# Optimization experiments

Hardware: AMD Instinct MI355X
Metric: run time of the kernel (lower is better)

Reference implementation:

```python
import jax, jax.numpy as jnp
import numpy as np

N_HEADS, D_MODEL, D_HEAD = 16, 1024, 64
INIT_STD = 0.02


def setup_inputs() -> dict:
    key = jax.random.key(0)
    ks = jax.random.split(key, 5)
    x = jax.random.normal(ks[0], (4, 2048, D_MODEL), dtype=jnp.float32)
    W_Q = jax.random.normal(ks[1], (N_HEADS, D_MODEL, D_HEAD), dtype=jnp.float32) * INIT_STD
    W_K = jax.random.normal(ks[2], (N_HEADS, D_MODEL, D_HEAD), dtype=jnp.float32) * INIT_STD
    W_V = jax.random.normal(ks[3], (N_HEADS, D_MODEL, D_HEAD), dtype=jnp.float32) * INIT_STD
    W_O = jax.random.normal(ks[4], (N_HEADS, D_HEAD, D_MODEL), dtype=jnp.float32) * INIT_STD
    b_Q = jnp.zeros((N_HEADS, D_HEAD), dtype=jnp.float32)
    b_K = jnp.zeros((N_HEADS, D_HEAD), dtype=jnp.float32)
    b_V = jnp.zeros((N_HEADS, D_HEAD), dtype=jnp.float32)
    b_O = jnp.zeros((D_MODEL,), dtype=jnp.float32)
    return {"normalized_resid_pre": x, "W_Q": W_Q, "W_K": W_K, "W_V": W_V,
            "W_O": W_O, "b_Q": b_Q, "b_K": b_K, "b_V": b_V, "b_O": b_O}


def reference(normalized_resid_pre, W_Q, W_K, W_V, W_O, b_Q, b_K, b_V, b_O):
    x = normalized_resid_pre  # [b, s, d_model]
    q = jnp.einsum('bsm,hmd->bshd', x, W_Q) + b_Q  # [b, s, h, d_head]
    k = jnp.einsum('bsm,hmd->bshd', x, W_K) + b_K
    v = jnp.einsum('bsm,hmd->bshd', x, W_V) + b_V
    scores = jnp.einsum('bqhd,bkhd->bhqk', q, k) / jnp.sqrt(jnp.float32(D_HEAD))
    S = x.shape[1]
    causal = jnp.tril(jnp.ones((S, S), dtype=bool))  # keep key_pos <= query_pos
    scores = jnp.where(causal, scores, jnp.finfo(scores.dtype).min)
    pattern = jax.nn.softmax(scores, axis=-1)  # [b, h, q, k]
    z = jnp.einsum('bhqk,bkhd->bqhd', pattern, v)
    attn_out = jnp.einsum('bqhd,hdm->bqm', z, W_O) + b_O
    return attn_out
```

## Files before the change

kernel.cpp:

```cpp
#include <hip/hip_runtime.h>
#include <hip/hip_bf16.h>
#include <math.h>

typedef __bf16 bf16_t;
typedef bf16_t bf16x8 __attribute__((ext_vector_type(8)));
typedef float f32x4 __attribute__((ext_vector_type(4)));

#define BB 4
#define SS 2048
#define HH 16
#define DMODEL 1024
#define DHEAD 64

#define QSCALE 0.18033688011112042f

__device__ inline unsigned short f2bf(float f) {
    union { __hip_bfloat16 h; unsigned short u; } cvt;
    cvt.h = __float2bfloat16(f);
    return cvt.u;
}

__device__ __forceinline__ void gll16(const unsigned short* g, unsigned short* l) {
    __builtin_amdgcn_global_load_lds(
        (const __attribute__((address_space(1))) unsigned int*)(g),
        (__attribute__((address_space(3))) unsigned int*)(l), 16, 0, 0);
}


__global__ void pack_x(const float* __restrict__ x, unsigned short* __restrict__ xb) {
    int i = blockIdx.x * 256 + threadIdx.x;
    const float4 v = ((const float4*)x)[i];
    unsigned short o[4] = { f2bf(v.x), f2bf(v.y), f2bf(v.z), f2bf(v.w) };
    *(uint2*)(xb + 4 * (size_t)i) = *(uint2*)o;
}

__global__ void pack_wqkv(const float* __restrict__ wq, const float* __restrict__ wk,
                          const float* __restrict__ wv, unsigned short* __restrict__ out) {
    int idx = blockIdx.x * 256 + threadIdx.x;
    int k  = idx & 1023;
    int n  = idx >> 10;
    int mat = n >> 10;
    int n1 = n & 1023;
    int h = n1 >> 6, d = n1 & 63;
    const float* w = (mat == 0) ? wq : (mat == 1) ? wk : wv;
    out[idx] = f2bf(w[(h << 16) + (k << 6) + d]);
}

__global__ void pack_wo(const float* __restrict__ wo, unsigned short* __restrict__ out) {
    int idx = blockIdx.x * 256 + threadIdx.x;
    int k = idx & 1023, n = idx >> 10;
    out[idx] = f2bf(wo[(k << 10) + n]);
}


__global__ __launch_bounds__(256) void gemm_qkv(
    const unsigned short* __restrict__ xb,
    const unsigned short* __restrict__ wT,
    const float* __restrict__ bq, const float* __restrict__ bk, const float* __restrict__ bv,
    unsigned short* __restrict__ qws, unsigned short* __restrict__ kws,
    unsigned short* __restrict__ vtw)
{
    __shared__ __align__(16) unsigned short lA[128 * 32];
    __shared__ __align__(16) unsigned short lB[128 * 32];
    const int t = threadIdx.x;
    const int lane = t & 63;
    const int w = t >> 6;
    const int quad = lane >> 4;
    const int l15 = lane & 15;
    const int n0 = blockIdx.x * 128;
    const int m0 = blockIdx.y * 128;
    const int wm = (w >> 1) * 64;
    const int wn = (w & 1) * 64;
    const int mat = n0 >> 10;

    f32x4 acc[4][4] = {};

    const int srow = w * 16 + (lane >> 2);
    const int scol = (lane & 3) * 8;
    const unsigned short* Ag0 = xb + (size_t)(m0 + srow) * 1024 + scol;
    const unsigned short* Ag1 = Ag0 + (size_t)64 * 1024;
    const unsigned short* Bg0 = wT + (size_t)(n0 + srow) * 1024 + scol;
    const unsigned short* Bg1 = Bg0 + (size_t)64 * 1024;
    unsigned short* lA0 = lA + (w * 16) * 32;
    unsigned short* lA1 = lA + (64 + w * 16) * 32;
    unsigned short* lB0 = lB + (w * 16) * 32;
    unsigned short* lB1 = lB + (64 + w * 16) * 32;

    if (mat != 2) {
        for (int kt = 0; kt < 1024; kt += 32) {
            __syncthreads();
            gll16(Ag0 + kt, lA0);
            gll16(Ag1 + kt, lA1);
            gll16(Bg0 + kt, lB0);
            gll16(Bg1 + kt, lB1);
            __syncthreads();
            bf16x8 af[4], bfr[4];
#pragma unroll
            for (int i = 0; i < 4; i++) {
                af[i]  = *(const bf16x8*)(lA + (wm + i * 16 + l15) * 32 + quad * 8);
                bfr[i] = *(const bf16x8*)(lB + (wn + i * 16 + l15) * 32 + quad * 8);
            }
#pragma unroll
            for (int i = 0; i < 4; i++)
#pragma unroll
                for (int j = 0; j < 4; j++)
                    acc[i][j] = __builtin_amdgcn_mfma_f32_16x16x32_bf16(bfr[j], af[i], acc[i][j], 0, 0, 0);
        }
        const int b = m0 >> 11;
        const float* bias_p = (mat == 0) ? bq : bk;
        const float scale = (mat == 0) ? QSCALE : 1.0f;
        unsigned short* dst = (mat == 0) ? qws : kws;
#pragma unroll
        for (int j = 0; j < 4; j++) {
            const int noff = wn + j * 16 + quad * 4;
            const int h = noff >> 6;
            const int hglob = ((n0 & 1023) >> 6) + h;
            const int dbase = noff & 63;
            const float4 bv4 = *(const float4*)(bias_p + hglob * 64 + dbase);
            const float bias_r[4] = { bv4.x, bv4.y, bv4.z, bv4.w };
#pragma unroll
            for (int i = 0; i < 4; i++) {
                const int s = (m0 & 2047) + wm + i * 16 + l15;
                unsigned short pk[4];
#pragma unroll
                for (int r = 0; r < 4; r++) pk[r] = f2bf((acc[i][j][r] + bias_r[r]) * scale);
                *(uint2*)(dst + (size_t)((b * 16 + hglob) * 2048 + s) * 64 + dbase) = *(uint2*)pk;
            }
        }
    } else {
        for (int kt = 0; kt < 1024; kt += 32) {
            __syncthreads();
            gll16(Ag0 + kt, lA0);
            gll16(Ag1 + kt, lA1);
            gll16(Bg0 + kt, lB0);
            gll16(Bg1 + kt, lB1);
            __syncthreads();
            bf16x8 af[4], bfr[4];
#pragma unroll
            for (int i = 0; i < 4; i++) {
                af[i]  = *(const bf16x8*)(lA + (wm + i * 16 + l15) * 32 + quad * 8);
                bfr[i] = *(const bf16x8*)(lB + (wn + i * 16 + l15) * 32 + quad * 8);
            }
#pragma unroll
            for (int i = 0; i < 4; i++)
#pragma unroll
                for (int j = 0; j < 4; j++)
                    acc[i][j] = __builtin_amdgcn_mfma_f32_16x16x32_bf16(af[i], bfr[j], acc[i][j], 0, 0, 0);
        }
        const int b = m0 >> 11;
#pragma unroll
        for (int j = 0; j < 4; j++) {
            const int n1 = (n0 & 1023) + wn + j * 16 + l15;
            const int h = n1 >> 6, d = n1 & 63;
            const float bias = bv[h * 64 + d];
#pragma unroll
            for (int i = 0; i < 4; i++) {
                const int s0 = (m0 & 2047) + wm + i * 16 + quad * 4;
                unsigned short pk[4];
#pragma unroll
                for (int r = 0; r < 4; r++) pk[r] = f2bf(acc[i][j][r] + bias);
                *(uint2*)(vtw + ((size_t)(b * 16 + h) * 64 + d) * 2048 + s0) = *(uint2*)pk;
            }
        }
    }
}


__global__ __launch_bounds__(256) void attn3(
    const unsigned short* __restrict__ qws,
    const unsigned short* __restrict__ kws,
    const unsigned short* __restrict__ vtw,
    unsigned short* __restrict__ zb)
{
    __shared__ __align__(16) unsigned short Ks[64 * 64];
    __shared__ __align__(16) unsigned short Vs[64 * 64];
    __shared__ __align__(16) unsigned short Ps[4 * 16 * 64];

    const int t = threadIdx.x;
    const int lane = t & 63;
    const int w = t >> 6;
    const int quad = lane >> 4;
    const int l15 = lane & 15;
    const int hi = l15 >> 3;
    const int lo = l15 & 7;

    const int qt = 31 - (blockIdx.x >> 6);
    const int bh = blockIdx.x & 63;
    const int q0 = qt * 64;
    const int qbase = q0 + w * 16;
    const size_t base = (size_t)bh * SS * DHEAD;
    const unsigned short* Q = qws + base;
    const unsigned short* K = kws + base;
    const unsigned short* Vt = vtw + base;

    bf16x8 qf0 = *(const bf16x8*)(Q + (size_t)(qbase + l15) * 64 + quad * 8);
    bf16x8 qf1 = *(const bf16x8*)(Q + (size_t)(qbase + l15) * 64 + 32 + quad * 8);

    f32x4 o[4] = {};
    float lsum[4] = {0.f, 0.f, 0.f, 0.f};
    unsigned short* Pw = Ps + w * 16 * 64;

    const int sr = t >> 2;
    const int g0 = t & 3;
    const int sw0 = ((g0 ^ (sr & 7)) << 3);
    const int sw1 = (((g0 + 4) ^ (sr & 7)) << 3);
    unsigned short* ksw = Ks + sr * 64;
    unsigned short* vsw = Vs + sr * 64;
    const unsigned short* Kg = K + (size_t)sr * 64 + g0 * 8;
    const unsigned short* Vg = Vt + (size_t)sr * 2048 + g0 * 8;

    const int gq0 = ((quad ^ lo) << 3);
    const int gq1 = (((quad + 4) ^ lo) << 3);

    const int nch = qt + 1;

    uint4 kr0 = *(const uint4*)(Kg);
    uint4 kr1 = *(const uint4*)(Kg + 32);
    uint4 vr0 = *(const uint4*)(Vg);
    uint4 vr1 = *(const uint4*)(Vg + 32);

    for (int c = 0; c < nch; c++) {
        __builtin_amdgcn_sched_barrier(0);
        __builtin_amdgcn_s_barrier();
        *(uint4*)(ksw + sw0) = kr0;
        *(uint4*)(ksw + sw1) = kr1;
        *(uint4*)(vsw + sw0) = vr0;
        *(uint4*)(vsw + sw1) = vr1;
        if (c + 1 < nch) {
            const unsigned short* kp = Kg + (size_t)(c + 1) * 64 * 64;
            const unsigned short* vp = Vg + (size_t)(c + 1) * 64;
            kr0 = *(const uint4*)(kp);
            kr1 = *(const uint4*)(kp + 32);
            vr0 = *(const uint4*)(vp);
            vr1 = *(const uint4*)(vp + 32);
        }
        asm volatile("s_waitcnt lgkmcnt(0)" ::: "memory");
        __builtin_amdgcn_s_barrier();
        __builtin_amdgcn_sched_barrier(0);

        f32x4 s[4];
        __builtin_amdgcn_s_setprio(1);
#pragma unroll
        for (int sub = 0; sub < 4; sub++) {
            const unsigned short* kr = Ks + (sub * 16 + l15) * 64;
            bf16x8 kf0 = *(const bf16x8*)(kr + gq0);
            bf16x8 kf1 = *(const bf16x8*)(kr + gq1);
            f32x4 sv = {};
            sv = __builtin_amdgcn_mfma_f32_16x16x32_bf16(qf0, kf0, sv, 0, 0, 0);
            sv = __builtin_amdgcn_mfma_f32_16x16x32_bf16(qf1, kf1, sv, 0, 0, 0);
            s[sub] = sv;
        }
        __builtin_amdgcn_s_setprio(0);

        const int kb = c * 64;
        if (c == nch - 1) {
            const int qg = qbase + quad * 4;
#pragma unroll
            for (int sub = 0; sub < 4; sub++) {
                const int key = kb + sub * 16 + l15;
#pragma unroll
                for (int r = 0; r < 4; r++) {
                    float p = (key > qg + r) ? 0.f : exp2f(s[sub][r]);
                    lsum[r] += p;
                    const int q = quad * 4 + r;
                    Pw[q * 64 + (((sub * 2 + hi) ^ (q & 7)) << 3) + lo] = f2bf(p);
                }
            }
        } else {
#pragma unroll
            for (int sub = 0; sub < 4; sub++)
#pragma unroll
                for (int r = 0; r < 4; r++) {
                    float p = exp2f(s[sub][r]);
                    lsum[r] += p;
                    const int q = quad * 4 + r;
                    Pw[q * 64 + (((sub * 2 + hi) ^ (q & 7)) << 3) + lo] = f2bf(p);
                }
        }
        asm volatile("s_waitcnt lgkmcnt(0)" ::: "memory");
        bf16x8 pf0 = *(const bf16x8*)(Pw + l15 * 64 + gq0);
        bf16x8 pf1 = *(const bf16x8*)(Pw + l15 * 64 + gq1);
        __builtin_amdgcn_s_setprio(1);
#pragma unroll
        for (int dt = 0; dt < 4; dt++) {
            const unsigned short* vrp = Vs + (dt * 16 + l15) * 64;
            bf16x8 vf0 = *(const bf16x8*)(vrp + gq0);
            bf16x8 vf1 = *(const bf16x8*)(vrp + gq1);
            o[dt] = __builtin_amdgcn_mfma_f32_16x16x32_bf16(vf0, pf0, o[dt], 0, 0, 0);
            o[dt] = __builtin_amdgcn_mfma_f32_16x16x32_bf16(vf1, pf1, o[dt], 0, 0, 0);
        }
        __builtin_amdgcn_s_setprio(0);
    }

#pragma unroll
    for (int r = 0; r < 4; r++) {
        float v = lsum[r];
        v += __shfl_xor(v, 1);
        v += __shfl_xor(v, 2);
        v += __shfl_xor(v, 4);
        v += __shfl_xor(v, 8);
        lsum[r] = v;
    }
    const int srcl = (l15 >> 2) << 4;
    float t0 = __shfl(lsum[0], srcl);
    float t1 = __shfl(lsum[1], srcl);
    float t2 = __shfl(lsum[2], srcl);
    float t3 = __shfl(lsum[3], srcl);
    const int rr = l15 & 3;
    float den = (rr == 0) ? t0 : (rr == 1) ? t1 : (rr == 2) ? t2 : t3;
    const float inv = 1.0f / den;

    const int b = bh >> 4, h = bh & 15;
    const int q = qbase + l15;
    unsigned short* zrow = zb + (size_t)(b * 2048 + q) * 1024 + h * 64 + quad * 4;
#pragma unroll
    for (int dt = 0; dt < 4; dt++) {
        unsigned short pk[4];
#pragma unroll
        for (int r = 0; r < 4; r++) pk[r] = f2bf(o[dt][r] * inv);
        *(uint2*)(zrow + dt * 16) = *(uint2*)pk;
    }
}


__global__ __launch_bounds__(256) void gemm_out(
    const unsigned short* __restrict__ zb,
    const unsigned short* __restrict__ wT,
    const float* __restrict__ bo,
    float* __restrict__ out)
{
    __shared__ __align__(16) unsigned short lA[128 * 32];
    __shared__ __align__(16) unsigned short lB[128 * 32];
    const int t = threadIdx.x;
    const int lane = t & 63;
    const int w = t >> 6;
    const int quad = lane >> 4;
    const int l15 = lane & 15;
    const int n0 = blockIdx.x * 128;
    const int m0 = blockIdx.y * 128;
    const int wm = (w >> 1) * 64;
    const int wn = (w & 1) * 64;

    f32x4 acc[4][4] = {};

    const int srow = w * 16 + (lane >> 2);
    const int scol = (lane & 3) * 8;
    const unsigned short* Ag0 = zb + (size_t)(m0 + srow) * 1024 + scol;
    const unsigned short* Ag1 = Ag0 + (size_t)64 * 1024;
    const unsigned short* Bg0 = wT + (size_t)(n0 + srow) * 1024 + scol;
    const unsigned short* Bg1 = Bg0 + (size_t)64 * 1024;
    unsigned short* lA0 = lA + (w * 16) * 32;
    unsigned short* lA1 = lA + (64 + w * 16) * 32;
    unsigned short* lB0 = lB + (w * 16) * 32;
    unsigned short* lB1 = lB + (64 + w * 16) * 32;

    for (int kt = 0; kt < 1024; kt += 32) {
        __syncthreads();
        gll16(Ag0 + kt, lA0);
        gll16(Ag1 + kt, lA1);
        gll16(Bg0 + kt, lB0);
        gll16(Bg1 + kt, lB1);
        __syncthreads();
        bf16x8 af[4], bfr[4];
#pragma unroll
        for (int i = 0; i < 4; i++) {
            af[i]  = *(const bf16x8*)(lA + (wm + i * 16 + l15) * 32 + quad * 8);
            bfr[i] = *(const bf16x8*)(lB + (wn + i * 16 + l15) * 32 + quad * 8);
        }
#pragma unroll
        for (int i = 0; i < 4; i++)
#pragma unroll
            for (int j = 0; j < 4; j++)
                acc[i][j] = __builtin_amdgcn_mfma_f32_16x16x32_bf16(bfr[j], af[i], acc[i][j], 0, 0, 0);
    }

#pragma unroll
    for (int j = 0; j < 4; j++) {
        const int nbase = n0 + wn + j * 16 + quad * 4;
        const float4 bv4 = *(const float4*)(bo + nbase);
#pragma unroll
        for (int i = 0; i < 4; i++) {
            const int s = m0 + wm + i * 16 + l15;
            float4 v;
            v.x = acc[i][j][0] + bv4.x;
            v.y = acc[i][j][1] + bv4.y;
            v.z = acc[i][j][2] + bv4.z;
            v.w = acc[i][j][3] + bv4.w;
            *(float4*)(out + (size_t)s * 1024 + nbase) = v;
        }
    }
}


extern "C" void kernel_launch(void* const* d_in, const int* in_sizes, int n_in,
                              void* d_out, int out_size, void* d_ws, size_t ws_size,
                              hipStream_t stream) {
    const float* x  = (const float*)d_in[0];
    const float* WQ = (const float*)d_in[1];
    const float* WK = (const float*)d_in[2];
    const float* WV = (const float*)d_in[3];
    const float* WO = (const float*)d_in[4];
    const float* bQ = (const float*)d_in[5];
    const float* bK = (const float*)d_in[6];
    const float* bV = (const float*)d_in[7];
    const float* bO = (const float*)d_in[8];
    float* out = (float*)d_out;

    char* ws = (char*)d_ws;
    unsigned short* xb   = (unsigned short*)ws;
    unsigned short* wqkv = (unsigned short*)(ws + (16u << 20));
    unsigned short* woT  = (unsigned short*)(ws + (22u << 20));
    unsigned short* qws  = (unsigned short*)(ws + (24u << 20));
    unsigned short* kws  = (unsigned short*)(ws + (40u << 20));
    unsigned short* vtw  = (unsigned short*)(ws + (56u << 20));
    unsigned short* zbuf = xb;

    pack_x<<<8192, 256, 0, stream>>>(x, xb);
    pack_wqkv<<<(3072 * 1024) / 256, 256, 0, stream>>>(WQ, WK, WV, wqkv);
    pack_wo<<<(1024 * 1024) / 256, 256, 0, stream>>>(WO, woT);
    gemm_qkv<<<dim3(24, 64), 256, 0, stream>>>(xb, wqkv, bQ, bK, bV, qws, kws, vtw);
    attn3<<<2048, 256, 0, stream>>>(qws, kws, vtw, zbuf);
    gemm_out<<<dim3(8, 64), 256, 0, stream>>>(zbuf, woT, bO, out);
}
```

Baseline: 303.3 us.

## Merge pack kernels with tiled transpose and transpose S in attention

Replaces the three separate bf16 pack kernels with a single launch. The weight transposes now go through a 64x64 shared-memory tile, so both the reads and writes are coalesced instead of scalar gathers. In attention, the QK^T MFMA operands are swapped so each lane holds one query row. This turns the P stores into 8-byte vector writes and shrinks the row-sum reduction to two cross-lane shuffles. The cost is more branching in the combined pack kernel and a new swizzle layout for P that has to stay consistent with the readback pattern.

```diff
diff --git a/kernel.cpp b/kernel.cpp
--- a/kernel.cpp
+++ b/kernel.cpp
@@ -27,29 +27,59 @@
 }
 
 
-__global__ void pack_x(const float* __restrict__ x, unsigned short* __restrict__ xb) {
-    int i = blockIdx.x * 256 + threadIdx.x;
-    const float4 v = ((const float4*)x)[i];
-    unsigned short o[4] = { f2bf(v.x), f2bf(v.y), f2bf(v.z), f2bf(v.w) };
-    *(uint2*)(xb + 4 * (size_t)i) = *(uint2*)o;
-}
-
-__global__ void pack_wqkv(const float* __restrict__ wq, const float* __restrict__ wk,
-                          const float* __restrict__ wv, unsigned short* __restrict__ out) {
-    int idx = blockIdx.x * 256 + threadIdx.x;
-    int k  = idx & 1023;
-    int n  = idx >> 10;
-    int mat = n >> 10;
-    int n1 = n & 1023;
-    int h = n1 >> 6, d = n1 & 63;
-    const float* w = (mat == 0) ? wq : (mat == 1) ? wk : wv;
-    out[idx] = f2bf(w[(h << 16) + (k << 6) + d]);
-}
-
-__global__ void pack_wo(const float* __restrict__ wo, unsigned short* __restrict__ out) {
-    int idx = blockIdx.x * 256 + threadIdx.x;
-    int k = idx & 1023, n = idx >> 10;
-    out[idx] = f2bf(wo[(k << 10) + n]);
+__global__ void pack_all(const float* __restrict__ x,
+                         const float* __restrict__ wq, const float* __restrict__ wk,
+                         const float* __restrict__ wv, const float* __restrict__ wo,
+                         unsigned short* __restrict__ xb, unsigned short* __restrict__ wqkv,
+                         unsigned short* __restrict__ woT) {
+    __shared__ float tile[64][65];
+    const int t = threadIdx.x;
+    const int bid = blockIdx.x;
+    if (bid < 8192) {
+        int i = bid * 256 + t;
+        const float4 v = ((const float4*)x)[i];
+        unsigned short o[4] = { f2bf(v.x), f2bf(v.y), f2bf(v.z), f2bf(v.w) };
+        *(uint2*)(xb + 4 * (size_t)i) = *(uint2*)o;
+        return;
+    }
+    const float* sbase;
+    int sstride;
+    unsigned short* dbase;
+    if (bid < 8192 + 768) {
+        int b2 = bid - 8192;
+        int mat = b2 >> 8, rem = b2 & 255;
+        int h = rem >> 4, mt = rem & 15;
+        const float* wsrc = (mat == 0) ? wq : (mat == 1) ? wk : wv;
+        sbase = wsrc + (h << 16) + ((mt * 64) << 6);
+        sstride = 64;
+        dbase = wqkv + (size_t)(mat * 1024 + h * 64) * 1024 + mt * 64;
+    } else {
+        int b3 = bid - 8960;
+        int kt = b3 >> 4, nt = b3 & 15;
+        sbase = wo + (size_t)(kt * 64) * 1024 + nt * 64;
+        sstride = 1024;
+        dbase = woT + (size_t)(nt * 64) * 1024 + kt * 64;
+    }
+    const int rr = t >> 4;
+    const int c4 = (t & 15) * 4;
+#pragma unroll
+    for (int i = 0; i < 4; i++) {
+        const int m = rr + 16 * i;
+        const float4 v = *(const float4*)(sbase + (size_t)m * sstride + c4);
+        tile[m][c4 + 0] = v.x;
+        tile[m][c4 + 1] = v.y;
+        tile[m][c4 + 2] = v.z;
+        tile[m][c4 + 3] = v.w;
+    }
+    __syncthreads();
+#pragma unroll
+    for (int i = 0; i < 4; i++) {
+        const int d = rr + 16 * i;
+        unsigned short pk[4];
+#pragma unroll
+        for (int j = 0; j < 4; j++) pk[j] = f2bf(tile[c4 + j][d]);
+        *(uint2*)(dbase + (size_t)d * 1024 + c4) = *(uint2*)pk;
+    }
 }
 
 
@@ -166,163 +196,6 @@
 }
 
 
-__global__ __launch_bounds__(256) void attn3(
-    const unsigned short* __restrict__ qws,
-    const unsigned short* __restrict__ kws,
-    const unsigned short* __restrict__ vtw,
-    unsigned short* __restrict__ zb)
-{
-    __shared__ __align__(16) unsigned short Ks[64 * 64];
-    __shared__ __align__(16) unsigned short Vs[64 * 64];
-    __shared__ __align__(16) unsigned short Ps[4 * 16 * 64];
-
-    const int t = threadIdx.x;
-    const int lane = t & 63;
-    const int w = t >> 6;
-    const int quad = lane >> 4;
-    const int l15 = lane & 15;
-    const int hi = l15 >> 3;
-    const int lo = l15 & 7;
-
-    const int qt = 31 - (blockIdx.x >> 6);
-    const int bh = blockIdx.x & 63;
-    const int q0 = qt * 64;
-    const int qbase = q0 + w * 16;
-    const size_t base = (size_t)bh * SS * DHEAD;
-    const unsigned short* Q = qws + base;
-    const unsigned short* K = kws + base;
-    const unsigned short* Vt = vtw + base;
-
-    bf16x8 qf0 = *(const bf16x8*)(Q + (size_t)(qbase + l15) * 64 + quad * 8);
-    bf16x8 qf1 = *(const bf16x8*)(Q + (size_t)(qbase + l15) * 64 + 32 + quad * 8);
-
-    f32x4 o[4] = {};
-    float lsum[4] = {0.f, 0.f, 0.f, 0.f};
-    unsigned short* Pw = Ps + w * 16 * 64;
-
-    const int sr = t >> 2;
-    const int g0 = t & 3;
-    const int sw0 = ((g0 ^ (sr & 7)) << 3);
-    const int sw1 = (((g0 + 4) ^ (sr & 7)) << 3);
-    unsigned short* ksw = Ks + sr * 64;
-    unsigned short* vsw = Vs + sr * 64;
-    const unsigned short* Kg = K + (size_t)sr * 64 + g0 * 8;
-    const unsigned short* Vg = Vt + (size_t)sr * 2048 + g0 * 8;
-
-    const int gq0 = ((quad ^ lo) << 3);
-    const int gq1 = (((quad + 4) ^ lo) << 3);
-
-    const int nch = qt + 1;
-
-    uint4 kr0 = *(const uint4*)(Kg);
-    uint4 kr1 = *(const uint4*)(Kg + 32);
-    uint4 vr0 = *(const uint4*)(Vg);
-    uint4 vr1 = *(const uint4*)(Vg + 32);
-
-    for (int c = 0; c < nch; c++) {
-        __builtin_amdgcn_sched_barrier(0);
-        __builtin_amdgcn_s_barrier();
-        *(uint4*)(ksw + sw0) = kr0;
-        *(uint4*)(ksw + sw1) = kr1;
-        *(uint4*)(vsw + sw0) = vr0;
-        *(uint4*)(vsw + sw1) = vr1;
-        if (c + 1 < nch) {
-            const unsigned short* kp = Kg + (size_t)(c + 1) * 64 * 64;
-            const unsigned short* vp = Vg + (size_t)(c + 1) * 64;
-            kr0 = *(const uint4*)(kp);
-            kr1 = *(const uint4*)(kp + 32);
-            vr0 = *(const uint4*)(vp);
-            vr1 = *(const uint4*)(vp + 32);
-        }
-        asm volatile("s_waitcnt lgkmcnt(0)" ::: "memory");
-        __builtin_amdgcn_s_barrier();
-        __builtin_amdgcn_sched_barrier(0);
-
-        f32x4 s[4];
-        __builtin_amdgcn_s_setprio(1);
-#pragma unroll
-        for (int sub = 0; sub < 4; sub++) {
-            const unsigned short* kr = Ks + (sub * 16 + l15) * 64;
-            bf16x8 kf0 = *(const bf16x8*)(kr + gq0);
-            bf16x8 kf1 = *(const bf16x8*)(kr + gq1);
-            f32x4 sv = {};
-            sv = __builtin_amdgcn_mfma_f32_16x16x32_bf16(qf0, kf0, sv, 0, 0, 0);
-            sv = __builtin_amdgcn_mfma_f32_16x16x32_bf16(qf1, kf1, sv, 0, 0, 0);
-            s[sub] = sv;
-        }
-        __builtin_amdgcn_s_setprio(0);
-
-        const int kb = c * 64;
-        if (c == nch - 1) {
-            const int qg = qbase + quad * 4;
-#pragma unroll
-            for (int sub = 0; sub < 4; sub++) {
-                const int key = kb + sub * 16 + l15;
-#pragma unroll
-                for (int r = 0; r < 4; r++) {
-                    float p = (key > qg + r) ? 0.f : exp2f(s[sub][r]);
-                    lsum[r] += p;
-                    const int q = quad * 4 + r;
-                    Pw[q * 64 + (((sub * 2 + hi) ^ (q & 7)) << 3) + lo] = f2bf(p);
-                }
-            }
-        } else {
-#pragma unroll
-            for (int sub = 0; sub < 4; sub++)
-#pragma unroll
-                for (int r = 0; r < 4; r++) {
-                    float p = exp2f(s[sub][r]);
-                    lsum[r] += p;
-                    const int q = quad * 4 + r;
-                    Pw[q * 64 + (((sub * 2 + hi) ^ (q & 7)) << 3) + lo] = f2bf(p);
-                }
-        }
-        asm volatile("s_waitcnt lgkmcnt(0)" ::: "memory");
-        bf16x8 pf0 = *(const bf16x8*)(Pw + l15 * 64 + gq0);
-        bf16x8 pf1 = *(const bf16x8*)(Pw + l15 * 64 + gq1);
-        __builtin_amdgcn_s_setprio(1);
-#pragma unroll
-        for (int dt = 0; dt < 4; dt++) {
-            const unsigned short* vrp = Vs + (dt * 16 + l15) * 64;
-            bf16x8 vf0 = *(const bf16x8*)(vrp + gq0);
-            bf16x8 vf1 = *(const bf16x8*)(vrp + gq1);
-            o[dt] = __builtin_amdgcn_mfma_f32_16x16x32_bf16(vf0, pf0, o[dt], 0, 0, 0);
-            o[dt] = __builtin_amdgcn_mfma_f32_16x16x32_bf16(vf1, pf1, o[dt], 0, 0, 0);
-        }
-        __builtin_amdgcn_s_setprio(0);
-    }
-
-#pragma unroll
-    for (int r = 0; r < 4; r++) {
-        float v = lsum[r];
-        v += __shfl_xor(v, 1);
-        v += __shfl_xor(v, 2);
-        v += __shfl_xor(v, 4);
-        v += __shfl_xor(v, 8);
-        lsum[r] = v;
-    }
-    const int srcl = (l15 >> 2) << 4;
-    float t0 = __shfl(lsum[0], srcl);
-    float t1 = __shfl(lsum[1], srcl);
-    float t2 = __shfl(lsum[2], srcl);
-    float t3 = __shfl(lsum[3], srcl);
-    const int rr = l15 & 3;
-    float den = (rr == 0) ? t0 : (rr == 1) ? t1 : (rr == 2) ? t2 : t3;
-    const float inv = 1.0f / den;
-
-    const int b = bh >> 4, h = bh & 15;
-    const int q = qbase + l15;
-    unsigned short* zrow = zb + (size_t)(b * 2048 + q) * 1024 + h * 64 + quad * 4;
-#pragma unroll
-    for (int dt = 0; dt < 4; dt++) {
-        unsigned short pk[4];
-#pragma unroll
-        for (int r = 0; r < 4; r++) pk[r] = f2bf(o[dt][r] * inv);
-        *(uint2*)(zrow + dt * 16) = *(uint2*)pk;
-    }
-}
-
-
 __global__ __launch_bounds__(256) void gemm_out(
     const unsigned short* __restrict__ zb,
     const unsigned short* __restrict__ wT,
@@ -392,6 +265,160 @@
 }
 
 
+__global__ __launch_bounds__(256) void attn3(
+    const unsigned short* __restrict__ qws,
+    const unsigned short* __restrict__ kws,
+    const unsigned short* __restrict__ vtw,
+    unsigned short* __restrict__ zb)
+{
+    __shared__ __align__(16) unsigned short Ks[64 * 64];
+    __shared__ __align__(16) unsigned short Vs[64 * 64];
+    __shared__ __align__(16) unsigned short Ps[4 * 16 * 64];
+
+    const int t = threadIdx.x;
+    const int lane = t & 63;
+    const int w = t >> 6;
+    const int quad = lane >> 4;
+    const int l15 = lane & 15;
+    const int lo = l15 & 7;
+
+    const int qt = 31 - (blockIdx.x >> 6);
+    const int bh = blockIdx.x & 63;
+    const int q0 = qt * 64;
+    const int qbase = q0 + w * 16;
+    const size_t base = (size_t)bh * SS * DHEAD;
+    const unsigned short* Q = qws + base;
+    const unsigned short* K = kws + base;
+    const unsigned short* Vt = vtw + base;
+
+    bf16x8 qf0 = *(const bf16x8*)(Q + (size_t)(qbase + l15) * 64 + quad * 8);
+    bf16x8 qf1 = *(const bf16x8*)(Q + (size_t)(qbase + l15) * 64 + 32 + quad * 8);
+
+    f32x4 o[4] = {};
+    float lsum = 0.f;
+    unsigned short* Pw = Ps + w * 16 * 64;
+
+    const int sr = t >> 2;
+    const int g0 = t & 3;
+    const int sw0 = ((g0 ^ (sr & 7)) << 3);
+    const int sw1 = (((g0 + 4) ^ (sr & 7)) << 3);
+    unsigned short* ksw = Ks + sr * 64;
+    unsigned short* vsw = Vs + sr * 64;
+    const unsigned short* Kg = K + (size_t)sr * 64 + g0 * 8;
+    const unsigned short* Vg = Vt + (size_t)sr * 2048 + g0 * 8;
+
+    const int gq0 = ((quad ^ lo) << 3);
+    const int gq1 = (((quad + 4) ^ lo) << 3);
+
+    unsigned short* pwr = Pw + l15 * 64;
+    unsigned short* pws0 = pwr + (((0 + quad) ^ (lo << 1)) << 2);
+    unsigned short* pws1 = pwr + (((4 + quad) ^ (lo << 1)) << 2);
+    unsigned short* pws2 = pwr + (((8 + quad) ^ (lo << 1)) << 2);
+    unsigned short* pws3 = pwr + (((12 + quad) ^ (lo << 1)) << 2);
+
+    const int nch = qt + 1;
+
+    uint4 kr0 = *(const uint4*)(Kg);
+    uint4 kr1 = *(const uint4*)(Kg + 32);
+    uint4 vr0 = *(const uint4*)(Vg);
+    uint4 vr1 = *(const uint4*)(Vg + 32);
+
+    for (int c = 0; c < nch; c++) {
+        __builtin_amdgcn_sched_barrier(0);
+        __builtin_amdgcn_s_barrier();
+        *(uint4*)(ksw + sw0) = kr0;
+        *(uint4*)(ksw + sw1) = kr1;
+        *(uint4*)(vsw + sw0) = vr0;
+        *(uint4*)(vsw + sw1) = vr1;
+        if (c + 1 < nch) {
+            const unsigned short* kp = Kg + (size_t)(c + 1) * 64 * 64;
+            const unsigned short* vp = Vg + (size_t)(c + 1) * 64;
+            kr0 = *(const uint4*)(kp);
+            kr1 = *(const uint4*)(kp + 32);
+            vr0 = *(const uint4*)(vp);
+            vr1 = *(const uint4*)(vp + 32);
+        }
+        asm volatile("s_waitcnt lgkmcnt(0)" ::: "memory");
+        __builtin_amdgcn_s_barrier();
+        __builtin_amdgcn_sched_barrier(0);
+
+        f32x4 s[4];
+        __builtin_amdgcn_s_setprio(1);
+#pragma unroll
+        for (int sub = 0; sub < 4; sub++) {
+            const unsigned short* kr = Ks + (sub * 16 + l15) * 64;
+            bf16x8 kf0 = *(const bf16x8*)(kr + gq0);
+            bf16x8 kf1 = *(const bf16x8*)(kr + gq1);
+            f32x4 sv = {};
+            sv = __builtin_amdgcn_mfma_f32_16x16x32_bf16(kf0, qf0, sv, 0, 0, 0);
+            sv = __builtin_amdgcn_mfma_f32_16x16x32_bf16(kf1, qf1, sv, 0, 0, 0);
+            s[sub] = sv;
+        }
+        __builtin_amdgcn_s_setprio(0);
+
+        const int kb = c * 64;
+        if (c == nch - 1) {
+            const int qg = qbase + l15;
+#pragma unroll
+            for (int sub = 0; sub < 4; sub++) {
+                const int k0 = kb + sub * 16 + quad * 4;
+                unsigned short pk[4];
+#pragma unroll
+                for (int r = 0; r < 4; r++) {
+                    float p = (k0 + r > qg) ? 0.f : exp2f(s[sub][r]);
+                    lsum += p;
+                    pk[r] = f2bf(p);
+                }
+                unsigned short* wp = (sub == 0) ? pws0 : (sub == 1) ? pws1 : (sub == 2) ? pws2 : pws3;
+                *(uint2*)wp = *(uint2*)pk;
+            }
+        } else {
+#pragma unroll
+            for (int sub = 0; sub < 4; sub++) {
+                unsigned short pk[4];
+#pragma unroll
+                for (int r = 0; r < 4; r++) {
+                    float p = exp2f(s[sub][r]);
+                    lsum += p;
+                    pk[r] = f2bf(p);
+                }
+                unsigned short* wp = (sub == 0) ? pws0 : (sub == 1) ? pws1 : (sub == 2) ? pws2 : pws3;
+                *(uint2*)wp = *(uint2*)pk;
+            }
+        }
+        asm volatile("s_waitcnt lgkmcnt(0)" ::: "memory");
+        bf16x8 pf0 = *(const bf16x8*)(Pw + l15 * 64 + gq0);
+        bf16x8 pf1 = *(const bf16x8*)(Pw + l15 * 64 + gq1);
+        __builtin_amdgcn_s_setprio(1);
+#pragma unroll
+        for (int dt = 0; dt < 4; dt++) {
+            const unsigned short* vrp = Vs + (dt * 16 + l15) * 64;
+            bf16x8 vf0 = *(const bf16x8*)(vrp + gq0);
+            bf16x8 vf1 = *(const bf16x8*)(vrp + gq1);
+            o[dt] = __builtin_amdgcn_mfma_f32_16x16x32_bf16(vf0, pf0, o[dt], 0, 0, 0);
+            o[dt] = __builtin_amdgcn_mfma_f32_16x16x32_bf16(vf1, pf1, o[dt], 0, 0, 0);
+        }
+        __builtin_amdgcn_s_setprio(0);
+    }
+
+    float v = lsum;
+    v += __shfl_xor(v, 16);
+    v += __shfl_xor(v, 32);
+    const float inv = 1.0f / v;
+
+    const int b = bh >> 4, h = bh & 15;
+    const int q = qbase + l15;
+    unsigned short* zrow = zb + (size_t)(b * 2048 + q) * 1024 + h * 64 + quad * 4;
+#pragma unroll
+    for (int dt = 0; dt < 4; dt++) {
+        unsigned short pk[4];
+#pragma unroll
+        for (int r = 0; r < 4; r++) pk[r] = f2bf(o[dt][r] * inv);
+        *(uint2*)(zrow + dt * 16) = *(uint2*)pk;
+    }
+}
+
+
 extern "C" void kernel_launch(void* const* d_in, const int* in_sizes, int n_in,
                               void* d_out, int out_size, void* d_ws, size_t ws_size,
                               hipStream_t stream) {
@@ -415,9 +442,7 @@
     unsigned short* vtw  = (unsigned short*)(ws + (56u << 20));
     unsigned short* zbuf = xb;
 
-    pack_x<<<8192, 256, 0, stream>>>(x, xb);
-    pack_wqkv<<<(3072 * 1024) / 256, 256, 0, stream>>>(WQ, WK, WV, wqkv);
-    pack_wo<<<(1024 * 1024) / 256, 256, 0, stream>>>(WO, woT);
+    pack_all<<<9216, 256, 0, stream>>>(x, WQ, WK, WV, WO, xb, wqkv, woT);
     gemm_qkv<<<dim3(24, 64), 256, 0, stream>>>(xb, wqkv, bQ, bK, bV, qws, kws, vtw);
     attn3<<<2048, 256, 0, stream>>>(qws, kws, vtw, zbuf);
     gemm_out<<<dim3(8, 64), 256, 0, stream>>>(zbuf, woT, bO, out);
```

Result: faster. 270.8 us (-10.7%).
